# Optimization experiments

Hardware: AMD Instinct MI355X
Metric: run time of the kernel (lower is better)

The kernel has to match this reference:

```python
import jax, jax.numpy as jnp
import numpy as np
from jax import lax

B = 64
HW = 72           # high-res grid hardcoded in the layer
LOW = 9           # 72 / stride 8
C = 3
N_ITERS = 200     # self._iterations
W_SCALE = 0.01    # keeps the FISTA operator contractive with random weights
DN = ('NHWC', 'HWIO', 'NHWC')


def setup_inputs() -> dict:
    key = jax.random.key(0)
    k1, k2, k3, k4 = jax.random.split(key, 4)
    x = jax.random.normal(k1, (B, LOW, LOW, C), jnp.float32)
    lam = jax.random.uniform(k2, (B,), jnp.float32)            # per-sample threshold
    w_conv = jax.random.normal(k3, (40, 40, C, C), jnp.float32) * W_SCALE  # Conv2D kernel
    b_conv = jnp.zeros((C,), jnp.float32)
    w_ct = jax.random.normal(k4, (5, 5, C, C), jnp.float32) * W_SCALE      # Conv2DTranspose kernel
    b_ct = jnp.zeros((C,), jnp.float32)
    return {"x": x, "lam": lam, "w_conv": w_conv, "b_conv": b_conv,
            "w_ct": w_ct, "b_ct": b_ct}


def reference(x, lam, w_conv, b_conv, w_ct, b_ct):
    lam4 = lam[:, None, None, None]  # (B,1,1,1) per-sample soft-threshold

    def A(y):  # Conv2D(3,(40,40),strides=8,'same'): (B,72,72,3)->(B,9,9,3)
        return lax.conv_general_dilated(y, w_conv, (8, 8), 'SAME',
                                        dimension_numbers=DN) + b_conv

    def At(r):  # Conv2DTranspose(3,(5,5),strides=8,'same'): (B,9,9,3)->(B,72,72,3)
        return lax.conv_transpose(r, w_ct, (8, 8), 'SAME',
                                  dimension_numbers=DN) + b_ct

    def softthresh(w):
        return jax.nn.relu(w - lam4) - jax.nn.relu(-w - lam4)

    def step(carry, _):
        y_tmp, y_last, t = carry
        re = At(x - A(y_tmp))
        w = y_tmp - re                      # mu = 1.0
        y_new = softthresh(w)
        t_n = (1.0 + jnp.sqrt(1.0 + 4.0 * t * t)) / 2.0
        y_tmp_next = y_new + (t - 1.0) / t_n * (y_new - y_last)
        return (y_tmp_next, y_new, t_n), None

    z = jnp.zeros((x.shape[0], HW, HW, C), x.dtype)
    init = (z, z, jnp.float32(1.0))
    (_, y_new, _), _ = lax.scan(step, init, None, length=N_ITERS)
    return y_new
```

## Files before the change

### kernel.cpp

```cpp
#include <hip/hip_runtime.h>
#include <math.h>


#define ITERS 200
#define THREADS 576
#define WGOFF 0
#define WCTOFF 19200
#define APOFF 19776
#define CNTOFF 144192
#define LY 0
#define LYL 3888
#define LA 7776
#define LXS 8020
#define LWG 8264
#define LWCT 14664
#define LT 15240
#define SMEMF 20100

template <int CTRL>
__device__ __forceinline__ float dpp_add(float x) {
  int moved = __builtin_amdgcn_update_dpp(0, __float_as_int(x), CTRL, 0xF, 0xF, true);
  return x + __int_as_float(moved);
}

__global__ void k0_init(const float* __restrict__ w_conv,
                        const float* __restrict__ w_ct,
                        float* __restrict__ ws) {
  const int i = blockIdx.x * 256 + threadIdx.x;
  if (i < 19200) {
    const int lane = i & 63;
    const int rest = i >> 6;
    const int g = rest / 75;
    const int tc = rest - 75 * g;
    const int t = tc / 3;
    const int co = tc - 3 * t;
    const int th = t / 5;
    const int tw = t - 5 * th;
    const int q = lane >> 4;
    const int pl = lane & 15;
    float v = 0.f;
    if (q < 3) {
      const int p = g * 16 + pl;
      const int ph = p >> 3;
      const int pw = p & 7;
      v = w_conv[(((8 * th + ph) * 40 + (8 * tw + pw)) * 3 + q) * 3 + co];
    }
    ws[WGOFF + i] = v;
  }
  if (i < 576) {
    const int ci = i % 3;
    const int r1 = i / 3;
    const int c = r1 % 3;
    const int r2 = r1 / 3;
    const int rw = r2 % 8;
    const int rh = r2 / 8;
    float v = 0.f;
    if (rh < 5 && rw < 5) v = w_ct[(((4 - rh) * 5 + (4 - rw)) * 3 + ci) * 3 + c];
    ws[WCTOFF + i] = v;
  }
  if (i < 4096) ((int*)ws)[CNTOFF + i] = 0;
}

__global__ __launch_bounds__(THREADS) void fista_split(
    float* __restrict__ ws,
    const float* __restrict__ x, const float* __restrict__ lam,
    const float* __restrict__ b_conv, const float* __restrict__ b_ct,
    float* __restrict__ out) {
  __shared__ __align__(16) float smem[SMEMF];
  const int tid = threadIdx.x;
  const int blk = blockIdx.x;
  const int n = blk & 63;
  const int g = blk >> 6;
  const int lane = tid & 63;
  const int wid = tid >> 6;
  const int q = lane >> 4;
  const int pl = lane & 15;
  const int ylane = ((q < 3) ? q : 2) * 16 + pl;
  const int oh = (wid == 0) ? 0 : (wid == 1) ? 4 : (wid == 4) ? 8
               : (wid == 8) ? 1 : wid;

  int* __restrict__ cnt = (int*)ws + CNTOFF + n * 64;
  const float lam_n = lam[n];
  const float bcv = b_conv[tid % 3];
  const float bct0 = b_ct[0], bct1 = b_ct[1], bct2 = b_ct[2];

  for (int i = tid; i < SMEMF; i += THREADS) smem[i] = 0.f;
  __syncthreads();
  for (int i = tid; i < 4800; i += THREADS) {
    const int lane_i = i & 63;
    const int tc = i >> 6;
    const int t_i = tc / 3;
    const int co_i = tc - 3 * t_i;
    smem[LWG + (t_i * 64 + lane_i) * 4 + co_i] = ws[WGOFF + g * 4800 + i];
  }
  smem[LWCT + tid] = ws[WCTOFF + tid];
  if (tid < 243) smem[LXS + tid] = x[n * 243 + tid];
  __syncthreads();

  const int idx3 = tid >> 1;
  const int cell = idx3 / 3;
  const int c = idx3 - 3 * cell;
  const int cb = 3 * cell;
  const int plb = (tid & 1) * 8;

  float t = 1.0f;
#pragma unroll 1
  for (int iter = 0; iter < ITERS; ++iter) {
    {
      float acc[27];
#pragma unroll
      for (int k = 0; k < 27; ++k) acc[k] = 0.f;

#pragma unroll
      for (int th = 0; th < 5; ++th) {
        const int r = oh + th - 2;
        if (r >= 0 && r <= 8) {
          float rv2[9];
#pragma unroll
          for (int wc = 0; wc < 9; ++wc)
            rv2[wc] = smem[LY + r * 432 + wc * 48 + ylane];

#pragma unroll
          for (int tw = 0; tw < 5; ++tw) {
            const float4 wv =
                *(const float4*)&smem[LWG + ((th * 5 + tw) * 64 + lane) * 4];
#pragma unroll
            for (int ow = 0; ow < 9; ++ow) {
              const int col = ow + tw - 2;
              if (col >= 0 && col <= 8) {
                const float y = rv2[col];
                acc[ow * 3 + 0] += y * wv.x;
                acc[ow * 3 + 1] += y * wv.y;
                acc[ow * 3 + 2] += y * wv.z;
              }
            }
          }
        }
      }

      float s4[27];
#pragma unroll
      for (int k = 0; k < 27; ++k) {
        const float s1 = dpp_add<0x111>(acc[k]);
        s4[k] = dpp_add<0x112>(s1);
      }
      {
        float* Tw = &smem[LT + wid * 540];
        if ((lane & 3) == 3) {
          const int m = lane >> 2;
#pragma unroll
          for (int k = 0; k < 27; ++k) Tw[k * 20 + m] = s4[k];
        }
        asm volatile("s_waitcnt lgkmcnt(0)" ::: "memory");
        if (lane < 27) {
          const float4* Tr = (const float4*)&Tw[lane * 20];
          const float4 p0 = Tr[0];
          const float4 p1 = Tr[1];
          const float4 p2 = Tr[2];
          const float4 p3 = Tr[3];
          const float s01 = (p0.x + p0.y) + (p0.z + p0.w);
          const float s23 = (p1.x + p1.y) + (p1.z + p1.w);
          const float s45 = (p2.x + p2.y) + (p2.z + p2.w);
          const float s67 = (p3.x + p3.y) + (p3.z + p3.w);
          const float s = (s01 + s23) + (s45 + s67);
          float* ap = ws + APOFF + ((((iter & 1) * 64 + n) * 4 + g) * 243)
                      + oh * 27 + lane;
          __hip_atomic_store(ap, s, __ATOMIC_RELAXED, __HIP_MEMORY_SCOPE_AGENT);
        }
      }
    }

    __syncthreads();
    if (tid == 0) {
      __hip_atomic_fetch_add(cnt, 1, __ATOMIC_RELAXED, __HIP_MEMORY_SCOPE_AGENT);
      const int target = 4 * (iter + 1);
      while (__hip_atomic_load(cnt, __ATOMIC_RELAXED, __HIP_MEMORY_SCOPE_AGENT)
             < target)
        __builtin_amdgcn_s_sleep(1);
    }
    __syncthreads();

    if (tid < 243) {
      const float* ap = ws + APOFF + ((iter & 1) * 64 + n) * 972;
      const float a0 = __hip_atomic_load(ap + tid, __ATOMIC_RELAXED,
                                         __HIP_MEMORY_SCOPE_AGENT);
      const float a1 = __hip_atomic_load(ap + 243 + tid, __ATOMIC_RELAXED,
                                         __HIP_MEMORY_SCOPE_AGENT);
      const float a2 = __hip_atomic_load(ap + 486 + tid, __ATOMIC_RELAXED,
                                         __HIP_MEMORY_SCOPE_AGENT);
      const float a3 = __hip_atomic_load(ap + 729 + tid, __ATOMIC_RELAXED,
                                         __HIP_MEMORY_SCOPE_AGENT);
      smem[LA + tid] = a0 + a1 + a2 + a3 + bcv;
    }
    __syncthreads();

    const float tn = (1.0f + sqrtf(1.0f + 4.0f * t * t)) * 0.5f;
    const float beta = (t - 1.0f) / tn;
    t = tn;

    const bool lastit = (iter == ITERS - 1);
    if (tid < 486) {
      const float a0 = smem[LA + cb + 0];
      const float a1 = smem[LA + cb + 1];
      const float a2 = smem[LA + cb + 2];
      const float r0 = smem[LXS + cb + 0] - a0;
      const float r1 = smem[LXS + cb + 1] - a1;
      const float r2v = smem[LXS + cb + 2] - a2;
      const float bct = (c == 0) ? bct0 : ((c == 1) ? bct1 : bct2);

      float4* lyv  = (float4*)&smem[LY];
      float4* lylv = (float4*)&smem[LYL];
      const float4 y0 = lyv[2 * tid];
      const float4 y1 = lyv[2 * tid + 1];
      const float yv[8] = {y0.x, y0.y, y0.z, y0.w, y1.x, y1.y, y1.z, y1.w};
      float yn[8];
#pragma unroll
      for (int j = 0; j < 8; ++j) {
        const int p = g * 16 + plb + j;
        const float* wp = &smem[LWCT + (p * 3 + c) * 3];
        const float re = bct + r0 * wp[0] + r1 * wp[1] + r2v * wp[2];
        const float wvv = yv[j] - re;
        yn[j] = fmaxf(wvv - lam_n, 0.f) - fmaxf(-wvv - lam_n, 0.f);
      }

      if (!lastit) {
        const float4 l0 = lylv[2 * tid];
        const float4 l1 = lylv[2 * tid + 1];
        const float ylv[8] = {l0.x, l0.y, l0.z, l0.w, l1.x, l1.y, l1.z, l1.w};
        float4 s0, s1, m0, m1;
        s0.x = yn[0]; s0.y = yn[1]; s0.z = yn[2]; s0.w = yn[3];
        s1.x = yn[4]; s1.y = yn[5]; s1.z = yn[6]; s1.w = yn[7];
        m0.x = yn[0] + beta * (yn[0] - ylv[0]);
        m0.y = yn[1] + beta * (yn[1] - ylv[1]);
        m0.z = yn[2] + beta * (yn[2] - ylv[2]);
        m0.w = yn[3] + beta * (yn[3] - ylv[3]);
        m1.x = yn[4] + beta * (yn[4] - ylv[4]);
        m1.y = yn[5] + beta * (yn[5] - ylv[5]);
        m1.z = yn[6] + beta * (yn[6] - ylv[6]);
        m1.w = yn[7] + beta * (yn[7] - ylv[7]);
        lylv[2 * tid] = s0; lylv[2 * tid + 1] = s1;
        lyv[2 * tid]  = m0; lyv[2 * tid + 1]  = m1;
      } else {
        const int part = (g * 16 + plb) >> 3;
        const int qh = cell / 9;
        const int qw = cell - 9 * qh;
        const int ih = 8 * qh + part;
        float* op = out + ((n * 72 + ih) * 72 + 8 * qw) * 3 + c;
#pragma unroll
        for (int j = 0; j < 8; ++j) op[3 * j] = yn[j];
      }
    }
    __syncthreads();
  }
}

extern "C" void kernel_launch(void* const* d_in, const int* in_sizes, int n_in,
                              void* d_out, int out_size, void* d_ws, size_t ws_size,
                              hipStream_t stream) {
  const float* x      = (const float*)d_in[0];
  const float* lam    = (const float*)d_in[1];
  const float* w_conv = (const float*)d_in[2];
  const float* b_conv = (const float*)d_in[3];
  const float* w_ct   = (const float*)d_in[4];
  const float* b_ct   = (const float*)d_in[5];
  float* out = (float*)d_out;
  float* ws  = (float*)d_ws;

  hipLaunchKernelGGL(k0_init, dim3(80), dim3(256), 0, stream, w_conv, w_ct, ws);
  hipLaunchKernelGGL(fista_split, dim3(256), dim3(THREADS), 0, stream,
                     ws, x, lam, b_conv, b_ct, out);
}
```

Baseline: 992.4 us.

## Keep conv weights in registers and prefetch update operands before grid barrier

```diff
diff --git a/kernel.cpp b/kernel.cpp
--- a/kernel.cpp
+++ b/kernel.cpp
@@ -12,10 +12,9 @@
 #define LYL 3888
 #define LA 7776
 #define LXS 8020
-#define LWG 8264
-#define LWCT 14664
-#define LT 15240
-#define SMEMF 20100
+#define LWCT 8264
+#define LT 8840
+#define SMEMF 20608
 
 template <int CTRL>
 __device__ __forceinline__ float dpp_add(float x) {
@@ -48,12 +47,11 @@
     ws[WGOFF + i] = v;
   }
   if (i < 576) {
-    const int ci = i % 3;
-    const int r1 = i / 3;
-    const int c = r1 % 3;
-    const int r2 = r1 / 3;
-    const int rw = r2 % 8;
-    const int rh = r2 / 8;
+    const int p = i & 63;
+    const int ci = (i >> 6) % 3;
+    const int c = i / 192;
+    const int rh = p >> 3;
+    const int rw = p & 7;
     float v = 0.f;
     if (rh < 5 && rw < 5) v = w_ct[(((4 - rh) * 5 + (4 - rw)) * 3 + ci) * 3 + c];
     ws[WCTOFF + i] = v;
@@ -84,15 +82,17 @@
   const float bcv = b_conv[tid % 3];
   const float bct0 = b_ct[0], bct1 = b_ct[1], bct2 = b_ct[2];
 
+  float wr0[25], wr1[25], wr2[25];
+#pragma unroll
+  for (int t5 = 0; t5 < 25; ++t5) {
+    const float* wb = ws + WGOFF + g * 4800 + t5 * 192 + lane;
+    wr0[t5] = wb[0];
+    wr1[t5] = wb[64];
+    wr2[t5] = wb[128];
+  }
+
   for (int i = tid; i < SMEMF; i += THREADS) smem[i] = 0.f;
   __syncthreads();
-  for (int i = tid; i < 4800; i += THREADS) {
-    const int lane_i = i & 63;
-    const int tc = i >> 6;
-    const int t_i = tc / 3;
-    const int co_i = tc - 3 * t_i;
-    smem[LWG + (t_i * 64 + lane_i) * 4 + co_i] = ws[WGOFF + g * 4800 + i];
-  }
   smem[LWCT + tid] = ws[WCTOFF + tid];
   if (tid < 243) smem[LXS + tid] = x[n * 243 + tid];
   __syncthreads();
@@ -102,6 +102,7 @@
   const int c = idx3 - 3 * cell;
   const int cb = 3 * cell;
   const int plb = (tid & 1) * 8;
+  const int pb = g * 16 + plb;
 
   float t = 1.0f;
 #pragma unroll 1
@@ -122,16 +123,18 @@
 
 #pragma unroll
           for (int tw = 0; tw < 5; ++tw) {
-            const float4 wv =
-                *(const float4*)&smem[LWG + ((th * 5 + tw) * 64 + lane) * 4];
+            const int t5 = th * 5 + tw;
+            const float w0 = wr0[t5];
+            const float w1 = wr1[t5];
+            const float w2 = wr2[t5];
 #pragma unroll
             for (int ow = 0; ow < 9; ++ow) {
               const int col = ow + tw - 2;
               if (col >= 0 && col <= 8) {
                 const float y = rv2[col];
-                acc[ow * 3 + 0] += y * wv.x;
-                acc[ow * 3 + 1] += y * wv.y;
-                acc[ow * 3 + 2] += y * wv.z;
+                acc[ow * 3 + 0] += y * w0;
+                acc[ow * 3 + 1] += y * w1;
+                acc[ow * 3 + 2] += y * w2;
               }
             }
           }
@@ -170,6 +173,21 @@
       }
     }
 
+    float4 py0 = {}, py1 = {}, pq0 = {}, pq1 = {};
+    float4 w0a = {}, w0b = {}, w1a = {}, w1b = {}, w2a = {}, w2b = {};
+    if (tid < 486) {
+      float4* lyv  = (float4*)&smem[LY];
+      float4* lylv = (float4*)&smem[LYL];
+      py0 = lyv[2 * tid];  py1 = lyv[2 * tid + 1];
+      pq0 = lylv[2 * tid]; pq1 = lylv[2 * tid + 1];
+      w0a = *(const float4*)&smem[LWCT + c * 192 +   0 + pb];
+      w0b = *(const float4*)&smem[LWCT + c * 192 +   4 + pb];
+      w1a = *(const float4*)&smem[LWCT + c * 192 +  64 + pb];
+      w1b = *(const float4*)&smem[LWCT + c * 192 +  68 + pb];
+      w2a = *(const float4*)&smem[LWCT + c * 192 + 128 + pb];
+      w2b = *(const float4*)&smem[LWCT + c * 192 + 132 + pb];
+    }
+
     __syncthreads();
     if (tid == 0) {
       __hip_atomic_fetch_add(cnt, 1, __ATOMIC_RELAXED, __HIP_MEMORY_SCOPE_AGENT);
@@ -190,7 +208,7 @@
                                          __HIP_MEMORY_SCOPE_AGENT);
       const float a3 = __hip_atomic_load(ap + 729 + tid, __ATOMIC_RELAXED,
                                          __HIP_MEMORY_SCOPE_AGENT);
-      smem[LA + tid] = a0 + a1 + a2 + a3 + bcv;
+      smem[LA + tid] = smem[LXS + tid] - (a0 + a1 + a2 + a3 + bcv);
     }
     __syncthreads();
 
@@ -200,33 +218,27 @@
 
     const bool lastit = (iter == ITERS - 1);
     if (tid < 486) {
-      const float a0 = smem[LA + cb + 0];
-      const float a1 = smem[LA + cb + 1];
-      const float a2 = smem[LA + cb + 2];
-      const float r0 = smem[LXS + cb + 0] - a0;
-      const float r1 = smem[LXS + cb + 1] - a1;
-      const float r2v = smem[LXS + cb + 2] - a2;
+      const float r0  = smem[LA + cb + 0];
+      const float r1  = smem[LA + cb + 1];
+      const float r2v = smem[LA + cb + 2];
       const float bct = (c == 0) ? bct0 : ((c == 1) ? bct1 : bct2);
+
+      const float wct0[8] = {w0a.x, w0a.y, w0a.z, w0a.w, w0b.x, w0b.y, w0b.z, w0b.w};
+      const float wct1[8] = {w1a.x, w1a.y, w1a.z, w1a.w, w1b.x, w1b.y, w1b.z, w1b.w};
+      const float wct2[8] = {w2a.x, w2a.y, w2a.z, w2a.w, w2b.x, w2b.y, w2b.z, w2b.w};
+      const float yv[8]   = {py0.x, py0.y, py0.z, py0.w, py1.x, py1.y, py1.z, py1.w};
+      float yn[8];
+#pragma unroll
+      for (int j = 0; j < 8; ++j) {
+        const float re = bct + r0 * wct0[j] + r1 * wct1[j] + r2v * wct2[j];
+        const float wvv = yv[j] - re;
+        yn[j] = fmaxf(wvv - lam_n, 0.f) - fmaxf(-wvv - lam_n, 0.f);
+      }
 
       float4* lyv  = (float4*)&smem[LY];
       float4* lylv = (float4*)&smem[LYL];
-      const float4 y0 = lyv[2 * tid];
-      const float4 y1 = lyv[2 * tid + 1];
-      const float yv[8] = {y0.x, y0.y, y0.z, y0.w, y1.x, y1.y, y1.z, y1.w};
-      float yn[8];
-#pragma unroll
-      for (int j = 0; j < 8; ++j) {
-        const int p = g * 16 + plb + j;
-        const float* wp = &smem[LWCT + (p * 3 + c) * 3];
-        const float re = bct + r0 * wp[0] + r1 * wp[1] + r2v * wp[2];
-        const float wvv = yv[j] - re;
-        yn[j] = fmaxf(wvv - lam_n, 0.f) - fmaxf(-wvv - lam_n, 0.f);
-      }
-
       if (!lastit) {
-        const float4 l0 = lylv[2 * tid];
-        const float4 l1 = lylv[2 * tid + 1];
-        const float ylv[8] = {l0.x, l0.y, l0.z, l0.w, l1.x, l1.y, l1.z, l1.w};
+        const float ylv[8] = {pq0.x, pq0.y, pq0.z, pq0.w, pq1.x, pq1.y, pq1.z, pq1.w};
         float4 s0, s1, m0, m1;
         s0.x = yn[0]; s0.y = yn[1]; s0.z = yn[2]; s0.w = yn[3];
         s1.x = yn[4]; s1.y = yn[5]; s1.z = yn[6]; s1.w = yn[7];
@@ -241,7 +253,7 @@
         lylv[2 * tid] = s0; lylv[2 * tid + 1] = s1;
         lyv[2 * tid]  = m0; lyv[2 * tid + 1]  = m1;
       } else {
-        const int part = (g * 16 + plb) >> 3;
+        const int part = pb >> 3;
         const int qh = cell / 9;
         const int qw = cell - 9 * qh;
         const int ih = 8 * qh + part;
```

New measurement: 2.752 ms. +177.3%, slower.
